# Kernel optimization log

Measured on AMD Instinct MI355X. Metric: run time of the kernel, lower is better.

The kernel has to match this reference:

```python
import jax, jax.numpy as jnp
import numpy as np

ALPHA = 1.0
BETA = 6.0
GAMMA = 1.0
N_DATA = 50000
IS_MSS = True
LOG2PI = float(np.log(2.0 * np.pi))


def _log_density_gaussian(x, mu, logvar):
    # elementwise Gaussian log-density
    return -0.5 * (LOG2PI + logvar) - 0.5 * (x - mu) ** 2 * jnp.exp(-logvar)


def _log_importance_weight_matrix(batch_size, n_data):
    # Faithful to the reference torch implementation (incl. the column-1 and
    # [M-1,0] stratified-weight overwrites done via flat strided assignment).
    N = float(n_data)
    M = float(batch_size - 1)
    strat = (N - M) / (N * M)
    W = jnp.full((batch_size, batch_size), 1.0 / M, dtype=jnp.float32)
    idx = jnp.arange(batch_size)
    W = W.at[idx, idx].set(1.0 / N)
    W = W.at[:, 1].set(strat)
    W = W.at[batch_size - 2, 0].set(strat)
    return jnp.log(W)


def setup_inputs() -> dict:
    key = jax.random.key(0)
    k1, k2, k3, k4, k5 = jax.random.split(key, 5)
    B, D = 1024, 64
    return {
        "recon_x": jax.random.normal(k1, (B, 3, 64, 64), dtype=jnp.float32),
        "x": jax.random.normal(k2, (B, 3, 64, 64), dtype=jnp.float32),
        "mu": jax.random.normal(k3, (B, D), dtype=jnp.float32),
        "logvar": jax.random.normal(k4, (B, D), dtype=jnp.float32),
        "noise": jax.random.normal(k5, (B, D), dtype=jnp.float32),
    }


def reference(recon_x, x, mu, logvar, noise):
    B, D = mu.shape
    # reconstruction: MSE with sum reduction
    reconstruction_loss = jnp.sum((recon_x - x) ** 2)

    # reparameterized latent sample (noise supplied deterministically)
    z = mu + noise * jnp.exp(0.5 * logvar)

    # log q(z|x) and log p(z), each summed over latent dims -> [B]
    log_q_zCx = _log_density_gaussian(z, mu, logvar).sum(axis=1)
    log_pz = _log_density_gaussian(z, jnp.zeros_like(z), jnp.zeros_like(z)).sum(axis=1)

    # pairwise matrix log q(z_i | x_j): [B, B, D]
    mat_log_qz = _log_density_gaussian(z[:, None, :], mu[None, :, :], logvar[None, :, :])
    if IS_MSS:
        log_iw = _log_importance_weight_matrix(B, N_DATA)
        mat_log_qz = mat_log_qz + log_iw[:, :, None]

    log_qz = jax.scipy.special.logsumexp(mat_log_qz.sum(axis=2), axis=1)  # [B]
    log_prod_qzi = jax.scipy.special.logsumexp(mat_log_qz, axis=1).sum(axis=1)  # [B]

    mi_loss = jnp.mean(log_q_zCx - log_qz)
    tc_loss = jnp.mean(log_qz - log_prod_qzi)
    dw_kl_loss = jnp.mean(log_prod_qzi - log_pz)

    return reconstruction_loss + (ALPHA * mi_loss + BETA * tc_loss + GAMMA * dw_kl_loss)
```

## Files before the change

### kernel.cpp

```cpp
#include <hip/hip_runtime.h>
#include <math.h>

typedef __attribute__((ext_vector_type(8))) short short8;
typedef __attribute__((ext_vector_type(4))) float f32x4;

#define BB 1024
#define DD 64
#define NPIX (1024*3*64*64)

#define LN2PI_F  1.8378770664093453f
#define LOG2E_F  1.4426950408889634f

#define INV_M  (1.0f/1023.0f)
#define INV_N  (1.0f/50000.0f)
#define STRATF ((float)((50000.0-1023.0)/(50000.0*1023.0)))
#define NEGBIG (-3.0e38f)

#define L2_INVM  (-9.9985904f)
#define L2_INVN  (-15.6096405f)
#define L2_STRAT (-10.0284195f)

#define WS_RP    0
#define WS_LQC   2048
#define WS_LPZ   3072
#define WS_LQZ   4096
#define WS_LPR   5120
#define WS_Z     6144
#define WS_Z2    71680
#define WS_A     137216
#define WS_B     202752
#define WS_C     268288
#define WS_KC    333824
#define WS_QZP   334848
#define WS_SEDP  400384
#define WS_ABF   924672
#define WS_BBF   990208

#define RECON_CHUNK_BLOCKS 512
#define RECON_CHUNK_F4     1048576
#define RECON_CHUNK_THREADS (RECON_CHUNK_BLOCKS*256)
#define RECON_REPS 8

#define NB_PREP  256
#define NB_MM    256
#define NB_SED   1024
#define NB_POST  256

__device__ __forceinline__ float fexp2(float x){ return __builtin_amdgcn_exp2f(x); }
__device__ __forceinline__ float flog2(float x){ return __builtin_amdgcn_logf(x); }
__device__ __forceinline__ unsigned short tobf(float f){
    unsigned int u = __float_as_uint(f);
    u = (u + 0x7FFFu + ((u >> 16) & 1u)) >> 16;
    return (unsigned short)u;
}
__device__ __forceinline__ unsigned long long ld_agent(const unsigned long long* p) {
    return __hip_atomic_load(p, __ATOMIC_RELAXED, __HIP_MEMORY_SCOPE_AGENT);
}

__device__ __forceinline__ void do_recon(int chunk, int lb, int t,
                                         const unsigned long long* rp,
                                         const unsigned long long* xp,
                                         float* __restrict__ ws,
                                         float* __restrict__ red) {
    long long base4 = (long long)chunk * RECON_CHUNK_F4 + lb * 256 + t;
    float acc = 0.f;
    #pragma unroll
    for (int rep = 0; rep < RECON_REPS; rep++) {
        long long i2 = 2LL * (base4 + rep * RECON_CHUNK_THREADS);
        unsigned long long a0 = ld_agent(rp + i2);
        unsigned long long a1 = ld_agent(rp + i2 + 1);
        unsigned long long b0 = ld_agent(xp + i2);
        unsigned long long b1 = ld_agent(xp + i2 + 1);
        float d0 = __uint_as_float((unsigned)a0)         - __uint_as_float((unsigned)b0);
        float d1 = __uint_as_float((unsigned)(a0 >> 32)) - __uint_as_float((unsigned)(b0 >> 32));
        float d2 = __uint_as_float((unsigned)a1)         - __uint_as_float((unsigned)b1);
        float d3 = __uint_as_float((unsigned)(a1 >> 32)) - __uint_as_float((unsigned)(b1 >> 32));
        acc = fmaf(d0, d0, acc); acc = fmaf(d1, d1, acc);
        acc = fmaf(d2, d2, acc); acc = fmaf(d3, d3, acc);
    }
    red[t] = acc; __syncthreads();
    for (int o = 128; o > 0; o >>= 1) {
        if (t < o) red[t] += red[t + o];
        __syncthreads();
    }
    if (t == 0) ws[WS_RP + chunk * RECON_CHUNK_BLOCKS + lb] = red[0];
}

__device__ __forceinline__ void do_prep(int pb, int t,
                                        const float* __restrict__ mu,
                                        const float* __restrict__ logvar,
                                        const float* __restrict__ noise,
                                        float* __restrict__ ws) {
    int d = t & 63, w = t >> 6;
    int i = pb * 4 + w;
    int idx = i * 64 + d;
    float m = mu[idx], lvv = logvar[idx], n = noise[idx];
    float sh   = fexp2(0.5f * LOG2E_F * lvv);
    float z    = fmaf(n, sh, m);
    float eneg = fexp2(-LOG2E_F * lvv);
    float a = -0.5f * LOG2E_F * eneg;
    float b = -2.0f * a * m;
    float c = fmaf(a, m * m, -0.5f * LOG2E_F * (LN2PI_F + lvv));
    float z2 = z * z;
    ws[WS_Z  + idx] = z;  ws[WS_Z2 + idx] = z2;
    ws[WS_A  + idx] = a;  ws[WS_B  + idx] = b;  ws[WS_C + idx] = c;
    unsigned short* abf = (unsigned short*)(ws + WS_ABF);
    unsigned short* bbf = (unsigned short*)(ws + WS_BBF);
    abf[i * 128 + d]      = tobf(z2);
    abf[i * 128 + 64 + d] = tobf(z);
    bbf[i * 128 + d]      = tobf(a);
    bbf[i * 128 + 64 + d] = tobf(b);
    float lqc = -0.5f * (LN2PI_F + lvv + n * n);
    float lpz = -0.5f * (LN2PI_F + z2);
    float kc  = c;
    for (int off = 32; off > 0; off >>= 1) {
        lqc += __shfl_xor(lqc, off, 64);
        lpz += __shfl_xor(lpz, off, 64);
        kc  += __shfl_xor(kc,  off, 64);
    }
    if (d == 0) { ws[WS_LQC + i] = lqc; ws[WS_LPZ + i] = lpz; ws[WS_KC + i] = kc; }
}

__device__ __forceinline__ void do_mm(int mmid, int t, float* __restrict__ ws) {
    int lane = t & 63, w = t >> 6;
    const unsigned short* abf = (const unsigned short*)(ws + WS_ABF);
    const unsigned short* bbf = (const unsigned short*)(ws + WS_BBF);
    int i0 = (mmid & 15) * 64, j0 = (mmid >> 4) * 64;
    int lo = lane & 15, g = lane >> 4;
    int wi = (w >> 1) * 32, wj = (w & 1) * 32;
    f32x4 acc[2][2] = {};
    #pragma unroll
    for (int kk = 0; kk < 4; kk++) {
        short8 af[2], bfr[2];
        #pragma unroll
        for (int fy = 0; fy < 2; fy++)
            af[fy] = *(const short8*)&abf[(i0 + wi + fy * 16 + lo) * 128 + (kk * 4 + g) * 8];
        #pragma unroll
        for (int fx = 0; fx < 2; fx++)
            bfr[fx] = *(const short8*)&bbf[(j0 + wj + fx * 16 + lo) * 128 + (kk * 4 + g) * 8];
        #pragma unroll
        for (int fy = 0; fy < 2; fy++)
            #pragma unroll
            for (int fx = 0; fx < 2; fx++)
                acc[fy][fx] = __builtin_amdgcn_mfma_f32_16x16x32_bf16(af[fy], bfr[fx], acc[fy][fx], 0, 0, 0);
    }
    int jA = j0 + wj + lo;
    float kcv0 = ws[WS_KC + jA], kcv1 = ws[WS_KC + jA + 16];
    int pc = (j0 >> 5) + (w & 1);
    #pragma unroll
    for (int fy = 0; fy < 2; fy++) {
        #pragma unroll
        for (int r = 0; r < 4; r++) {
            int i = i0 + wi + fy * 16 + g * 4 + r;
            float vv0, vv1;
            {
                int j = jA;
                float lw = (j == 1) ? L2_STRAT : (i == j) ? L2_INVN
                         : (i == 1022 && j == 0) ? L2_STRAT : L2_INVM;
                vv0 = acc[fy][0][r] + kcv0 + 64.0f * lw;
            }
            {
                int j = jA + 16;
                float lw = (j == 1) ? L2_STRAT : (i == j) ? L2_INVN
                         : (i == 1022 && j == 0) ? L2_STRAT : L2_INVM;
                vv1 = acc[fy][1][r] + kcv1 + 64.0f * lw;
            }
            float m = fmaxf(vv0, vv1);
            float s = fexp2(vv0 - m) + fexp2(vv1 - m);
            for (int off = 1; off < 16; off <<= 1) {
                float om = __shfl_xor(m, off, 64);
                float os = __shfl_xor(s, off, 64);
                float M = fmaxf(m, om);
                s = s * fexp2(m - M) + os * fexp2(om - M);
                m = M;
            }
            if (lo == 0) {
                ws[WS_QZP + ((pc << 10) + i) * 2]     = m;
                ws[WS_QZP + ((pc << 10) + i) * 2 + 1] = s;
            }
        }
    }
}

__device__ __forceinline__ void do_sed(int sid, int t, float* __restrict__ ws,
                                       float* __restrict__ sacc) {
    int lane = t & 63, w = t >> 6;
    int ic = sid & 127, jc = sid >> 7;
    int i0 = ic * 8, d = lane;
    int jbase = jc * 128 + w * 32;
    const float* Ap = ws + WS_A;
    const float* Bp = ws + WS_B;
    const float* Cp = ws + WS_C;
    float z2r[8], zr[8], se[8];
    #pragma unroll
    for (int k = 0; k < 8; k++) {
        z2r[k] = ws[WS_Z2 + (i0 + k) * 64 + d];
        zr[k]  = ws[WS_Z  + (i0 + k) * 64 + d];
        se[k] = 0.f;
    }
    float aP[8], bP[8], cP[8], aQ[8], bQ[8], cQ[8];
    #pragma unroll
    for (int u = 0; u < 8; u++) {
        int gg = (jbase + u) * 64 + d;
        aP[u] = Ap[gg]; bP[u] = Bp[gg]; cP[u] = Cp[gg];
    }
    #pragma unroll
    for (int batch = 0; batch < 4; batch++) {
        if (batch < 3) {
            #pragma unroll
            for (int u = 0; u < 8; u++) {
                int gg = (jbase + (batch + 1) * 8 + u) * 64 + d;
                aQ[u] = Ap[gg]; bQ[u] = Bp[gg]; cQ[u] = Cp[gg];
            }
        }
        #pragma unroll
        for (int u = 0; u < 8; u++) {
            #pragma unroll
            for (int k = 0; k < 8; k++) {
                float uu = fmaf(aP[u], z2r[k], fmaf(bP[u], zr[k], cP[u]));
                se[k] += fexp2(uu);
            }
        }
        if (batch < 3) {
            #pragma unroll
            for (int u = 0; u < 8; u++) { aP[u] = aQ[u]; bP[u] = bQ[u]; cP[u] = cQ[u]; }
        }
    }
    #pragma unroll
    for (int k = 0; k < 8; k++) sacc[w * 512 + k * 64 + d] = se[k];
    __syncthreads();
    int k0 = w * 2;
    for (int k = k0; k < k0 + 2; k++) {
        float tot = sacc[k * 64 + d] + sacc[512 + k * 64 + d]
                  + sacc[1024 + k * 64 + d] + sacc[1536 + k * 64 + d];
        ws[WS_SEDP + ((jc << 10) + i0 + k) * 64 + d] = tot;
    }
}

__device__ __forceinline__ void do_post(int pb, int t, float* __restrict__ ws) {
    int lane = t & 63, w = t >> 6;
    int i = pb * 4 + w;
    float m = NEGBIG, s = 0.f;
    if (lane < 32) {
        m = ws[WS_QZP + ((lane << 10) + i) * 2];
        s = ws[WS_QZP + ((lane << 10) + i) * 2 + 1];
    }
    for (int off = 1; off < 64; off <<= 1) {
        float om = __shfl_xor(m, off, 64);
        float os = __shfl_xor(s, off, 64);
        float M = fmaxf(m, om);
        s = s * fexp2(m - M) + os * fexp2(om - M);
        m = M;
    }
    if (lane == 0) ws[WS_LQZ + i] = (m + flog2(s)) * (1.0f / LOG2E_F);
    int d = lane;
    float se = 0.f;
    for (int c = 0; c < 8; c++) se += ws[WS_SEDP + ((c << 10) + i) * 64 + d];
    float z2 = ws[WS_Z2 + i * 64 + d], z = ws[WS_Z + i * 64 + d];
    auto E = [&](int j) -> float {
        int gidx = j * 64 + d;
        return fexp2(fmaf(ws[WS_A + gidx], z2, fmaf(ws[WS_B + gidx], z, ws[WS_C + gidx])));
    };
    float sid = INV_M * se;
    if (i != 1)    sid += (INV_N  - INV_M) * E(i);
    sid += (STRATF - INV_M) * E(1);
    if (i == 1022) sid += (STRATF - INV_M) * E(0);
    float lg = flog2(sid);
    for (int off = 1; off < 64; off <<= 1) lg += __shfl_xor(lg, off, 64);
    if (d == 0) ws[WS_LPR + i] = lg * (1.0f / LOG2E_F);
}

__global__ __launch_bounds__(256) void k_d1(const float* __restrict__ rx,
                                            const float* __restrict__ x,
                                            const float* __restrict__ mu,
                                            const float* __restrict__ logvar,
                                            const float* __restrict__ noise,
                                            float* __restrict__ ws) {
    __shared__ float smem[256];
    int bid = blockIdx.x, t = threadIdx.x;
    if (bid < RECON_CHUNK_BLOCKS)
        do_recon(0, bid, t, (const unsigned long long*)rx, (const unsigned long long*)x, ws, smem);
    else
        do_prep(bid - RECON_CHUNK_BLOCKS, t, mu, logvar, noise, ws);
}

__global__ __launch_bounds__(256) void k_d2(const float* __restrict__ rx,
                                            const float* __restrict__ x,
                                            float* __restrict__ ws) {
    __shared__ float smem[2048];
    int bid = blockIdx.x, t = threadIdx.x;
    if (bid < RECON_CHUNK_BLOCKS)
        do_recon(1, bid, t, (const unsigned long long*)rx, (const unsigned long long*)x, ws, smem);
    else if (bid < RECON_CHUNK_BLOCKS + NB_MM)
        do_mm(bid - RECON_CHUNK_BLOCKS, t, ws);
    else
        do_sed(bid - RECON_CHUNK_BLOCKS - NB_MM, t, ws, smem);
}

__global__ __launch_bounds__(256) void k_d3(const float* __restrict__ rx,
                                            const float* __restrict__ x,
                                            float* __restrict__ ws) {
    __shared__ float smem[256];
    int bid = blockIdx.x, t = threadIdx.x;
    if (bid < RECON_CHUNK_BLOCKS)
        do_recon(2, bid, t, (const unsigned long long*)rx, (const unsigned long long*)x, ws, smem);
    else
        do_post(bid - RECON_CHUNK_BLOCKS, t, ws);
}

__global__ __launch_bounds__(256) void k_final(const float* __restrict__ ws,
                                               float* __restrict__ out) {
    int t = threadIdx.x;
    float a0 = 0, a1 = 0, a2 = 0, a3 = 0, a4 = 0;
    for (int idx = t; idx < 1536; idx += 256) a0 += ws[WS_RP + idx];
    for (int idx = t; idx < BB; idx += 256) {
        a1 += ws[WS_LQC + idx];
        a2 += ws[WS_LPZ + idx];
        a3 += ws[WS_LQZ + idx];
        a4 += ws[WS_LPR + idx];
    }
    __shared__ float red[256];
    float vals[5] = {a0, a1, a2, a3, a4};
    float res[5];
    for (int q = 0; q < 5; q++) {
        red[t] = vals[q]; __syncthreads();
        for (int o = 128; o > 0; o >>= 1) {
            if (t < o) red[t] += red[t + o];
            __syncthreads();
        }
        res[q] = red[0]; __syncthreads();
    }
    if (t == 0) {
        float recon = res[0], slqc = res[1], slpz = res[2], slqz = res[3], slpr = res[4];
        out[0] = recon + (slqc + 5.f * (slqz - slpr) - slpz) * (1.0f / (float)BB);
    }
}

extern "C" void kernel_launch(void* const* d_in, const int* in_sizes, int n_in,
                              void* d_out, int out_size, void* d_ws, size_t ws_size,
                              hipStream_t stream) {
    (void)in_sizes; (void)n_in; (void)out_size; (void)ws_size;
    const float* rx = (const float*)d_in[0];
    const float* x  = (const float*)d_in[1];
    const float* mu = (const float*)d_in[2];
    const float* lv = (const float*)d_in[3];
    const float* nz = (const float*)d_in[4];
    float* ws  = (float*)d_ws;
    float* out = (float*)d_out;

    k_d1   <<<RECON_CHUNK_BLOCKS + NB_PREP,          256, 0, stream>>>(rx, x, mu, lv, nz, ws);
    k_d2   <<<RECON_CHUNK_BLOCKS + NB_MM + NB_SED,   256, 0, stream>>>(rx, x, ws);
    k_d3   <<<RECON_CHUNK_BLOCKS + NB_POST,          256, 0, stream>>>(rx, x, ws);
    k_final<<<1, 256, 0, stream>>>(ws, out);
}
```

Before: 45.30 us.

## Fuse per-dimension logsumexp finalization into full-width SED blocks and reorder block dispatch

The SED stage now has 128 blocks, each covering all 1024 j values for 8 rows, instead of 1024 blocks covering 128-column chunks. That removes the SEDP partial buffer and lets each block apply the importance-weight corrections, take the log and reduce over d in place. Only the log_qz merge is left for the third kernel. Block order in each fused kernel is also flipped so the dependent compute blocks dispatch before the recon streaming blocks. The cost is less parallelism in the exp-heavy SED phase (128 long-running blocks instead of 1024 short ones), which could leave it as a longer tail.

```diff
diff --git a/kernel.cpp b/kernel.cpp
--- a/kernel.cpp
+++ b/kernel.cpp
@@ -32,7 +32,6 @@
 #define WS_C     268288
 #define WS_KC    333824
 #define WS_QZP   334848
-#define WS_SEDP  400384
 #define WS_ABF   924672
 #define WS_BBF   990208
 
@@ -41,10 +40,10 @@
 #define RECON_CHUNK_THREADS (RECON_CHUNK_BLOCKS*256)
 #define RECON_REPS 8
 
-#define NB_PREP  256
-#define NB_MM    256
-#define NB_SED   1024
-#define NB_POST  256
+#define NB_PREP   256
+#define NB_MM     256
+#define NB_SEDF   128
+#define NB_POSTQZ 256
 
 __device__ __forceinline__ float fexp2(float x){ return __builtin_amdgcn_exp2f(x); }
 __device__ __forceinline__ float flog2(float x){ return __builtin_amdgcn_logf(x); }
@@ -182,12 +181,11 @@
     }
 }
 
-__device__ __forceinline__ void do_sed(int sid, int t, float* __restrict__ ws,
-                                       float* __restrict__ sacc) {
+__device__ __forceinline__ void do_sedfull(int sid, int t, float* __restrict__ ws,
+                                           float* __restrict__ sacc) {
     int lane = t & 63, w = t >> 6;
-    int ic = sid & 127, jc = sid >> 7;
-    int i0 = ic * 8, d = lane;
-    int jbase = jc * 128 + w * 32;
+    int i0 = sid * 8, d = lane;
+    int jbase = w * 256;
     const float* Ap = ws + WS_A;
     const float* Bp = ws + WS_B;
     const float* Cp = ws + WS_C;
@@ -204,9 +202,8 @@
         int gg = (jbase + u) * 64 + d;
         aP[u] = Ap[gg]; bP[u] = Bp[gg]; cP[u] = Cp[gg];
     }
-    #pragma unroll
-    for (int batch = 0; batch < 4; batch++) {
-        if (batch < 3) {
+    for (int batch = 0; batch < 32; batch++) {
+        if (batch < 31) {
             #pragma unroll
             for (int u = 0; u < 8; u++) {
                 int gg = (jbase + (batch + 1) * 8 + u) * 64 + d;
@@ -221,7 +218,7 @@
                 se[k] += fexp2(uu);
             }
         }
-        if (batch < 3) {
+        if (batch < 31) {
             #pragma unroll
             for (int u = 0; u < 8; u++) { aP[u] = aQ[u]; bP[u] = bQ[u]; cP[u] = cQ[u]; }
         }
@@ -229,15 +226,28 @@
     #pragma unroll
     for (int k = 0; k < 8; k++) sacc[w * 512 + k * 64 + d] = se[k];
     __syncthreads();
-    int k0 = w * 2;
-    for (int k = k0; k < k0 + 2; k++) {
+    #pragma unroll
+    for (int kq = 0; kq < 2; kq++) {
+        int k = w * 2 + kq;
+        int i = i0 + k;
         float tot = sacc[k * 64 + d] + sacc[512 + k * 64 + d]
                   + sacc[1024 + k * 64 + d] + sacc[1536 + k * 64 + d];
-        ws[WS_SEDP + ((jc << 10) + i0 + k) * 64 + d] = tot;
-    }
-}
-
-__device__ __forceinline__ void do_post(int pb, int t, float* __restrict__ ws) {
+        float z2 = z2r[k], z = zr[k];
+        auto E = [&](int j) -> float {
+            int gidx = j * 64 + d;
+            return fexp2(fmaf(Ap[gidx], z2, fmaf(Bp[gidx], z, Cp[gidx])));
+        };
+        float sidv = INV_M * tot;
+        if (i != 1)    sidv += (INV_N  - INV_M) * E(i);
+        sidv += (STRATF - INV_M) * E(1);
+        if (i == 1022) sidv += (STRATF - INV_M) * E(0);
+        float lg = flog2(sidv);
+        for (int off = 1; off < 64; off <<= 1) lg += __shfl_xor(lg, off, 64);
+        if (d == 0) ws[WS_LPR + i] = lg * (1.0f / LOG2E_F);
+    }
+}
+
+__device__ __forceinline__ void do_postqz(int pb, int t, float* __restrict__ ws) {
     int lane = t & 63, w = t >> 6;
     int i = pb * 4 + w;
     float m = NEGBIG, s = 0.f;
@@ -253,21 +263,6 @@
         m = M;
     }
     if (lane == 0) ws[WS_LQZ + i] = (m + flog2(s)) * (1.0f / LOG2E_F);
-    int d = lane;
-    float se = 0.f;
-    for (int c = 0; c < 8; c++) se += ws[WS_SEDP + ((c << 10) + i) * 64 + d];
-    float z2 = ws[WS_Z2 + i * 64 + d], z = ws[WS_Z + i * 64 + d];
-    auto E = [&](int j) -> float {
-        int gidx = j * 64 + d;
-        return fexp2(fmaf(ws[WS_A + gidx], z2, fmaf(ws[WS_B + gidx], z, ws[WS_C + gidx])));
-    };
-    float sid = INV_M * se;
-    if (i != 1)    sid += (INV_N  - INV_M) * E(i);
-    sid += (STRATF - INV_M) * E(1);
-    if (i == 1022) sid += (STRATF - INV_M) * E(0);
-    float lg = flog2(sid);
-    for (int off = 1; off < 64; off <<= 1) lg += __shfl_xor(lg, off, 64);
-    if (d == 0) ws[WS_LPR + i] = lg * (1.0f / LOG2E_F);
 }
 
 __global__ __launch_bounds__(256) void k_d1(const float* __restrict__ rx,
@@ -278,10 +273,10 @@
                                             float* __restrict__ ws) {
     __shared__ float smem[256];
     int bid = blockIdx.x, t = threadIdx.x;
-    if (bid < RECON_CHUNK_BLOCKS)
-        do_recon(0, bid, t, (const unsigned long long*)rx, (const unsigned long long*)x, ws, smem);
+    if (bid < NB_PREP)
+        do_prep(bid, t, mu, logvar, noise, ws);
     else
-        do_prep(bid - RECON_CHUNK_BLOCKS, t, mu, logvar, noise, ws);
+        do_recon(0, bid - NB_PREP, t, (const unsigned long long*)rx, (const unsigned long long*)x, ws, smem);
 }
 
 __global__ __launch_bounds__(256) void k_d2(const float* __restrict__ rx,
@@ -289,12 +284,12 @@
                                             float* __restrict__ ws) {
     __shared__ float smem[2048];
     int bid = blockIdx.x, t = threadIdx.x;
-    if (bid < RECON_CHUNK_BLOCKS)
-        do_recon(1, bid, t, (const unsigned long long*)rx, (const unsigned long long*)x, ws, smem);
-    else if (bid < RECON_CHUNK_BLOCKS + NB_MM)
-        do_mm(bid - RECON_CHUNK_BLOCKS, t, ws);
+    if (bid < NB_MM)
+        do_mm(bid, t, ws);
+    else if (bid < NB_MM + NB_SEDF)
+        do_sedfull(bid - NB_MM, t, ws, smem);
     else
-        do_sed(bid - RECON_CHUNK_BLOCKS - NB_MM, t, ws, smem);
+        do_recon(1, bid - NB_MM - NB_SEDF, t, (const unsigned long long*)rx, (const unsigned long long*)x, ws, smem);
 }
 
 __global__ __launch_bounds__(256) void k_d3(const float* __restrict__ rx,
@@ -302,10 +297,10 @@
                                             float* __restrict__ ws) {
     __shared__ float smem[256];
     int bid = blockIdx.x, t = threadIdx.x;
-    if (bid < RECON_CHUNK_BLOCKS)
-        do_recon(2, bid, t, (const unsigned long long*)rx, (const unsigned long long*)x, ws, smem);
+    if (bid < NB_POSTQZ)
+        do_postqz(bid, t, ws);
     else
-        do_post(bid - RECON_CHUNK_BLOCKS, t, ws);
+        do_recon(2, bid - NB_POSTQZ, t, (const unsigned long long*)rx, (const unsigned long long*)x, ws, smem);
 }
 
 __global__ __launch_bounds__(256) void k_final(const float* __restrict__ ws,
@@ -348,8 +343,8 @@
     float* ws  = (float*)d_ws;
     float* out = (float*)d_out;
 
-    k_d1   <<<RECON_CHUNK_BLOCKS + NB_PREP,          256, 0, stream>>>(rx, x, mu, lv, nz, ws);
-    k_d2   <<<RECON_CHUNK_BLOCKS + NB_MM + NB_SED,   256, 0, stream>>>(rx, x, ws);
-    k_d3   <<<RECON_CHUNK_BLOCKS + NB_POST,          256, 0, stream>>>(rx, x, ws);
+    k_d1   <<<NB_PREP + RECON_CHUNK_BLOCKS,            256, 0, stream>>>(rx, x, mu, lv, nz, ws);
+    k_d2   <<<NB_MM + NB_SEDF + RECON_CHUNK_BLOCKS,    256, 0, stream>>>(rx, x, ws);
+    k_d3   <<<NB_POSTQZ + RECON_CHUNK_BLOCKS,          256, 0, stream>>>(rx, x, ws);
     k_final<<<1, 256, 0, stream>>>(ws, out);
 }
```

New measurement: 63.68 us. 40.6% more time.
